# Performance work log

Measured on AMD Instinct MI355X. Metric: run time of the kernel, lower is better.

## Reference

```python
import jax, jax.numpy as jnp
import numpy as np

B, T, D, K = 32, 1024, 256, 1024


def setup_inputs() -> dict:
    key = jax.random.key(0)
    k1, k2 = jax.random.split(key)
    z_e_x = jax.random.normal(k1, (B, T, D), dtype=jnp.float32)
    # codebook initialized uniform(-1/K, 1/K) as in VQEmbedding.__init__
    codebook = jax.random.uniform(k2, (K, D), minval=-1.0 / K, maxval=1.0 / K, dtype=jnp.float32)
    return {"z_e_x": z_e_x, "codebook": codebook}


def _vq_indices(x_flat, codebook):
    c_sqr = jnp.sum(codebook * codebook, axis=1)            # [K]
    x_sqr = jnp.sum(x_flat * x_flat, axis=1, keepdims=True)  # [N,1]
    dist = c_sqr[None, :] + x_sqr - 2.0 * (x_flat @ codebook.T)  # [N,K]
    return jnp.argmin(dist, axis=1)                          # [N]


def reference(z_e_x, codebook):
    # VQEmbedding.straight_through with slice=1 (forward values)
    shp = z_e_x.shape
    x_flat = z_e_x.reshape(-1, codebook.shape[1])            # [N,D]
    idx = _vq_indices(x_flat, codebook)                      # [N] int
    codes = codebook[idx].reshape(shp)                       # gather lookup
    # z_q_x and z_q_x_bar are numerically identical (differ only in grad path);
    # also return the indices (what VQEmbedding.forward returns)
    return codes, codes, idx.reshape(shp[:-1])
```

## Files before the change

kernel.cpp:

```cpp
#include <hip/hip_runtime.h>


#define NROWS  32768
#define DDIM   256
#define KCODES 1024
#define MARGIN 1.5e-3f
#define CAP    1024
#define RPB    64
#define NCHUNK 16

typedef __attribute__((ext_vector_type(8))) short short8;
typedef __attribute__((ext_vector_type(4))) float f32x4;

__device__ __forceinline__ unsigned short f2bf(float f) {
    unsigned u = __float_as_uint(f);
    return (unsigned short)((u + 0x7FFFu + ((u >> 16) & 1u)) >> 16);
}

__device__ __forceinline__ float exact_dot(const float* __restrict__ xrow,
                                           const float* __restrict__ crow) {
    const float4* xp = (const float4*)xrow;
    const float4* cp = (const float4*)crow;
    float A = 0.f, B = 0.f;
    #pragma unroll 8
    for (int d4 = 0; d4 < 32; ++d4) {
        float4 xv = xp[d4], cv = cp[d4];
        A = __fmaf_rn(xv.x, cv.x, A);
        A = __fmaf_rn(xv.y, cv.y, A);
        A = __fmaf_rn(xv.z, cv.z, A);
        A = __fmaf_rn(xv.w, cv.w, A);
    }
    #pragma unroll 8
    for (int d4 = 32; d4 < 64; ++d4) {
        float4 xv = xp[d4], cv = cp[d4];
        B = __fmaf_rn(xv.x, cv.x, B);
        B = __fmaf_rn(xv.y, cv.y, B);
        B = __fmaf_rn(xv.z, cv.z, B);
        B = __fmaf_rn(xv.w, cv.w, B);
    }
    return __fadd_rn(A, B);
}

__global__ __launch_bounds__(256) void vq_csqr(const float* __restrict__ cb,
                                               float* __restrict__ csqr) {
    int gid  = blockIdx.x * 256 + threadIdx.x;
    int w    = gid >> 6;
    int lane = threadIdx.x & 63;
    if (w >= KCODES) return;
    float4 v = reinterpret_cast<const float4*>(cb)[w * (DDIM / 4) + lane];
    float s = v.x * v.x + v.y * v.y + v.z * v.z + v.w * v.w;
    #pragma unroll
    for (int off = 32; off > 0; off >>= 1) s += __shfl_down(s, off, 64);
    if (lane == 0) csqr[w] = s;
}

__global__ __launch_bounds__(256) void vq_xsqr(const float* __restrict__ x,
                                               float* __restrict__ xsqr) {
    int w = threadIdx.x >> 6, lane = threadIdx.x & 63;
    int row = blockIdx.x * 4 + w;
    float4 v = reinterpret_cast<const float4*>(x + (size_t)row * DDIM)[lane];
    float s = v.x * v.x + v.y * v.y + v.z * v.z + v.w * v.w;
    #pragma unroll
    for (int off = 32; off > 0; off >>= 1) s += __shfl_down(s, off, 64);
    if (lane == 0) xsqr[row] = s;
}

__global__ __launch_bounds__(256) void vq_cbfrag(const float* __restrict__ cb,
                                                 short* __restrict__ cbh) {
    int id   = blockIdx.x * 256 + threadIdx.x;
    int lane = id & 63;
    int ks   = (id >> 6) & 7;
    int nt   = id >> 9;
    int code = nt * 16 + (lane & 15);
    int d0   = ks * 32 + (lane >> 4) * 8;
    const float4* p = (const float4*)(cb + (size_t)code * DDIM + d0);
    float4 a = p[0], b = p[1];
    short8 v;
    v[0] = (short)f2bf(a.x); v[1] = (short)f2bf(a.y);
    v[2] = (short)f2bf(a.z); v[3] = (short)f2bf(a.w);
    v[4] = (short)f2bf(b.x); v[5] = (short)f2bf(b.y);
    v[6] = (short)f2bf(b.z); v[7] = (short)f2bf(b.w);
    *(short8*)(cbh + (size_t)id * 8) = v;
}

__global__ __launch_bounds__(256, 2) void vq_main(const float* __restrict__ x,
                                                  const float* __restrict__ cb,
                                                  const short* __restrict__ cbh,
                                                  const float* __restrict__ csqr,
                                                  const float* __restrict__ xsqr,
                                                  float* __restrict__ out) {
    __shared__ short              bstage[2][4 * 8 * 64 * 8];
    __shared__ float              csl[KCODES];
    __shared__ unsigned long long keys[RPB];
    __shared__ unsigned           list[CAP];
    __shared__ int                fidx[RPB];
    __shared__ int                cnt, ovf;

    const int t    = threadIdx.x;
    const int lane = t & 63;
    const int w    = t >> 6;
    const int r0   = blockIdx.x * RPB;
    const int lr   = lane & 15;
    const int lg   = lane >> 4;

    ((float4*)csl)[t] = ((const float4*)csqr)[t];
    if (t < RPB) keys[t] = ~0ULL;
    if (t == 0) { cnt = 0; ovf = 0; }

    short8 afr[8];
    {
        const float* xr = x + (size_t)(r0 + w * 16 + lr) * DDIM;
        #pragma unroll
        for (int ks = 0; ks < 8; ++ks) {
            float4 a = *(const float4*)&xr[ks * 32 + lg * 8];
            float4 b = *(const float4*)&xr[ks * 32 + lg * 8 + 4];
            short8 v;
            v[0] = (short)f2bf(a.x); v[1] = (short)f2bf(a.y);
            v[2] = (short)f2bf(a.z); v[3] = (short)f2bf(a.w);
            v[4] = (short)f2bf(b.x); v[5] = (short)f2bf(b.y);
            v[6] = (short)f2bf(b.z); v[7] = (short)f2bf(b.w);
            afr[ks] = v;
        }
    }

    const short8* cbh8 = (const short8*)cbh;

    short8 pf[8];
    #pragma unroll
    for (int i = 0; i < 8; ++i) pf[i] = cbh8[(size_t)0 * 2048 + i * 256 + t];
    {
        short8* dst = (short8*)bstage[0];
        #pragma unroll
        for (int i = 0; i < 8; ++i) dst[i * 256 + t] = pf[i];
        #pragma unroll
        for (int i = 0; i < 8; ++i) pf[i] = cbh8[(size_t)1 * 2048 + i * 256 + t];
    }
    __syncthreads();

    unsigned runp[4];
    #pragma unroll
    for (int j = 0; j < 4; ++j) runp[j] = ~0u;
    float thr[4];

    for (int c = 0; c < 2 * NCHUNK; ++c) {
        const int q = c & (NCHUNK - 1);
        if (c + 1 < 2 * NCHUNK) {
            short8* dst = (short8*)bstage[(c + 1) & 1];
            #pragma unroll
            for (int i = 0; i < 8; ++i) dst[i * 256 + t] = pf[i];
        }
        if (c + 2 < 2 * NCHUNK) {
            const size_t cb2 = (size_t)((c + 2) & (NCHUNK - 1)) * 2048;
            #pragma unroll
            for (int i = 0; i < 8; ++i) pf[i] = cbh8[cb2 + i * 256 + t];
        }
        const short* bs = bstage[c & 1];
        #pragma unroll
        for (int m = 0; m < 4; ++m) {
            const int nt = q * 4 + m;
            short8 bv[8];
            #pragma unroll
            for (int ks = 0; ks < 8; ++ks)
                bv[ks] = *(const short8*)&bs[((m * 8 + ks) * 64 + lane) * 8];
            f32x4 af = (f32x4){0.f, 0.f, 0.f, 0.f};
            #pragma unroll
            for (int ks = 0; ks < 8; ++ks)
                af = __builtin_amdgcn_mfma_f32_16x16x32_bf16(afr[ks], bv[ks], af, 0, 0, 0);

            const int code = nt * 16 + lr;
            float cs1 = __fadd_rn(csl[code], 1.0f);
            if (c < NCHUNK) {
                #pragma unroll
                for (int j = 0; j < 4; ++j) {
                    float s = __fmaf_rn(-2.f, af[j], cs1);
                    unsigned kp = (__float_as_uint(s) & 0xFFFFFC00u) | (unsigned)code;
                    runp[j] = runp[j] < kp ? runp[j] : kp;
                }
            } else {
                #pragma unroll
                for (int j = 0; j < 4; ++j) {
                    float s = __fmaf_rn(-2.f, af[j], cs1);
                    if (s <= thr[j]) {
                        int row = w * 16 + lg * 4 + j;
                        int pos = atomicAdd(&cnt, 1);
                        if (pos < CAP) list[pos] = ((unsigned)row << 10) | (unsigned)code;
                        else ovf = 1;
                    }
                }
            }
        }
        if (c == NCHUNK - 1) {
            #pragma unroll
            for (int j = 0; j < 4; ++j) {
                unsigned v = runp[j];
                #pragma unroll
                for (int mm = 1; mm < 16; mm <<= 1) {
                    unsigned o = __shfl_xor(v, mm, 64);
                    v = o < v ? o : v;
                }
                thr[j] = __uint_as_float(v & 0xFFFFFC00u) + MARGIN;
            }
        }
        __syncthreads();
    }

    if (ovf || cnt > CAP) {
        for (int it = t; it < RPB * KCODES; it += 256) {
            int row = it >> 10, code = it & (KCODES - 1);
            float dot = exact_dot(x + (size_t)(r0 + row) * DDIM, cb + (size_t)code * DDIM);
            float s   = __fmaf_rn(-2.f, dot, __fadd_rn(csl[code], xsqr[r0 + row]));
            atomicMin(&keys[row], ((unsigned long long)__float_as_uint(s) << 32) | (unsigned)code);
        }
    } else {
        for (int i = t; i < cnt; i += 256) {
            unsigned e = list[i];
            int row = (int)(e >> 10), code = (int)(e & 0x3FFu);
            float dot = exact_dot(x + (size_t)(r0 + row) * DDIM, cb + (size_t)code * DDIM);
            float s   = __fmaf_rn(-2.f, dot, __fadd_rn(csl[code], xsqr[r0 + row]));
            atomicMin(&keys[row], ((unsigned long long)__float_as_uint(s) << 32) | (unsigned)code);
        }
    }
    __syncthreads();

    if (t < RPB) {
        int code = (int)(unsigned)(keys[t] & 0xffffffffu);
        fidx[t] = code;
        out[(size_t)2 * NROWS * DDIM + (r0 + t)] = (float)code;
    }
    __syncthreads();

    const float4* cb4  = (const float4*)cb;
    float4*       out0 = (float4*)out;
    float4*       out1 = out0 + (size_t)NROWS * (DDIM / 4);
    #pragma unroll
    for (int i = 0; i < 16; ++i) {
        int it  = i * 256 + t;
        int row = it >> 6, col = it & 63;
        float4 v = cb4[(size_t)fidx[row] * (DDIM / 4) + col];
        size_t o = (size_t)(r0 + row) * (DDIM / 4) + col;
        out0[o] = v;
        out1[o] = v;
    }
}

extern "C" void kernel_launch(void* const* d_in, const int* in_sizes, int n_in,
                              void* d_out, int out_size, void* d_ws, size_t ws_size,
                              hipStream_t stream) {
    const float* x   = (const float*)d_in[0];
    const float* cb  = (const float*)d_in[1];
    float*       out = (float*)d_out;

    float* ws_csqr = (float*)d_ws;
    float* ws_xsqr = ws_csqr + KCODES;
    short* ws_cbh  = (short*)(ws_xsqr + NROWS);

    vq_cbfrag<<<128,        256, 0, stream>>>(cb, ws_cbh);
    vq_csqr  <<<256,        256, 0, stream>>>(cb, ws_csqr);
    vq_xsqr  <<<NROWS / 4,  256, 0, stream>>>(x, ws_xsqr);
    vq_main  <<<NROWS / RPB, 256, 0, stream>>>(x, cb, ws_cbh, ws_csqr, ws_xsqr, out);
}
```

Baseline: 94.05 us.

## Split codes across waves, hold all row tiles in registers, stage via global_load_lds

Each wave now keeps A fragments for all four 16-row tiles and handles its own quarter of the codebook, so every B fragment read from LDS feeds four MFMAs instead of one. Codebook staging uses direct global-to-LDS loads instead of round-tripping through registers. Because each wave only sees part of the codes, the running minimum becomes a cross-wave reduction through shared memory, with an extra barrier to build per-row thresholds. This raises register pressure (16 short8 A fragments plus 16 accumulators) and may limit occupancy.

After: 101.1 us. 7.5% more time.

```diff
diff --git a/kernel.cpp b/kernel.cpp
--- a/kernel.cpp
+++ b/kernel.cpp
@@ -91,6 +91,8 @@
                                                   float* __restrict__ out) {
     __shared__ short              bstage[2][4 * 8 * 64 * 8];
     __shared__ float              csl[KCODES];
+    __shared__ float              wred[4][RPB];
+    __shared__ float              thrl[RPB];
     __shared__ unsigned long long keys[RPB];
     __shared__ unsigned           list[CAP];
     __shared__ int                fidx[RPB];
@@ -107,9 +109,10 @@
     if (t < RPB) keys[t] = ~0ULL;
     if (t == 0) { cnt = 0; ovf = 0; }
 
-    short8 afr[8];
-    {
-        const float* xr = x + (size_t)(r0 + w * 16 + lr) * DDIM;
+    short8 afr[4][8];
+    #pragma unroll
+    for (int tile = 0; tile < 4; ++tile) {
+        const float* xr = x + (size_t)(r0 + tile * 16 + lr) * DDIM;
         #pragma unroll
         for (int ks = 0; ks < 8; ++ks) {
             float4 a = *(const float4*)&xr[ks * 32 + lg * 8];
@@ -119,89 +122,111 @@
             v[2] = (short)f2bf(a.z); v[3] = (short)f2bf(a.w);
             v[4] = (short)f2bf(b.x); v[5] = (short)f2bf(b.y);
             v[6] = (short)f2bf(b.z); v[7] = (short)f2bf(b.w);
-            afr[ks] = v;
-        }
-    }
-
-    const short8* cbh8 = (const short8*)cbh;
-
-    short8 pf[8];
-    #pragma unroll
-    for (int i = 0; i < 8; ++i) pf[i] = cbh8[(size_t)0 * 2048 + i * 256 + t];
-    {
-        short8* dst = (short8*)bstage[0];
-        #pragma unroll
-        for (int i = 0; i < 8; ++i) dst[i * 256 + t] = pf[i];
-        #pragma unroll
-        for (int i = 0; i < 8; ++i) pf[i] = cbh8[(size_t)1 * 2048 + i * 256 + t];
-    }
+            afr[tile][ks] = v;
+        }
+    }
+
+    const char* cbb = (const char*)cbh;
+    auto stage_chunk = [&](int buf, int c) {
+        const char* srcb = cbb + ((size_t)(w * 16 + c) << 13);
+        char*       dstb = (char*)bstage[buf] + ((size_t)w << 13);
+        #pragma unroll
+        for (int i = 0; i < 8; ++i) {
+            const void* src = srcb + i * 1024 + lane * 16;
+            __builtin_amdgcn_global_load_lds(
+                (const __attribute__((address_space(1))) void*)src,
+                (__attribute__((address_space(3))) void*)(dstb + i * 1024),
+                16, 0, 0);
+        }
+    };
+
+    stage_chunk(0, 0);
     __syncthreads();
 
-    unsigned runp[4];
-    #pragma unroll
-    for (int j = 0; j < 4; ++j) runp[j] = ~0u;
-    float thr[4];
-
-    for (int c = 0; c < 2 * NCHUNK; ++c) {
-        const int q = c & (NCHUNK - 1);
-        if (c + 1 < 2 * NCHUNK) {
-            short8* dst = (short8*)bstage[(c + 1) & 1];
-            #pragma unroll
-            for (int i = 0; i < 8; ++i) dst[i * 256 + t] = pf[i];
-        }
-        if (c + 2 < 2 * NCHUNK) {
-            const size_t cb2 = (size_t)((c + 2) & (NCHUNK - 1)) * 2048;
-            #pragma unroll
-            for (int i = 0; i < 8; ++i) pf[i] = cbh8[cb2 + i * 256 + t];
-        }
-        const short* bs = bstage[c & 1];
-        #pragma unroll
-        for (int m = 0; m < 4; ++m) {
-            const int nt = q * 4 + m;
-            short8 bv[8];
-            #pragma unroll
-            for (int ks = 0; ks < 8; ++ks)
-                bv[ks] = *(const short8*)&bs[((m * 8 + ks) * 64 + lane) * 8];
-            f32x4 af = (f32x4){0.f, 0.f, 0.f, 0.f};
-            #pragma unroll
-            for (int ks = 0; ks < 8; ++ks)
-                af = __builtin_amdgcn_mfma_f32_16x16x32_bf16(afr[ks], bv[ks], af, 0, 0, 0);
-
-            const int code = nt * 16 + lr;
-            float cs1 = __fadd_rn(csl[code], 1.0f);
-            if (c < NCHUNK) {
+    float runp[4][4];
+    #pragma unroll
+    for (int tile = 0; tile < 4; ++tile)
+        #pragma unroll
+        for (int j = 0; j < 4; ++j) runp[tile][j] = __builtin_inff();
+    float thr[4][4];
+
+    for (int cc = 0; cc < 2 * NCHUNK; ++cc) {
+        const int c = cc & (NCHUNK - 1);
+        if (cc + 1 < 2 * NCHUNK) stage_chunk((cc + 1) & 1, (cc + 1) & (NCHUNK - 1));
+
+        const short* bs = bstage[cc & 1];
+        short8 bv[8];
+        #pragma unroll
+        for (int ks = 0; ks < 8; ++ks)
+            bv[ks] = *(const short8*)&bs[((w * 8 + ks) * 64 + lane) * 8];
+        f32x4 af[4];
+        #pragma unroll
+        for (int tile = 0; tile < 4; ++tile) af[tile] = (f32x4){0.f, 0.f, 0.f, 0.f};
+        #pragma unroll
+        for (int ks = 0; ks < 8; ++ks) {
+            #pragma unroll
+            for (int tile = 0; tile < 4; ++tile)
+                af[tile] = __builtin_amdgcn_mfma_f32_16x16x32_bf16(afr[tile][ks], bv[ks], af[tile], 0, 0, 0);
+        }
+
+        const int nt   = w * 16 + c;
+        const int code = nt * 16 + lr;
+        const float cs1 = __fadd_rn(csl[code], 1.0f);
+        if (cc < NCHUNK) {
+            #pragma unroll
+            for (int tile = 0; tile < 4; ++tile)
                 #pragma unroll
                 for (int j = 0; j < 4; ++j) {
-                    float s = __fmaf_rn(-2.f, af[j], cs1);
-                    unsigned kp = (__float_as_uint(s) & 0xFFFFFC00u) | (unsigned)code;
-                    runp[j] = runp[j] < kp ? runp[j] : kp;
+                    float s = __fmaf_rn(-2.f, af[tile][j], cs1);
+                    runp[tile][j] = fminf(runp[tile][j], s);
                 }
-            } else {
+        } else {
+            #pragma unroll
+            for (int tile = 0; tile < 4; ++tile)
                 #pragma unroll
                 for (int j = 0; j < 4; ++j) {
-                    float s = __fmaf_rn(-2.f, af[j], cs1);
-                    if (s <= thr[j]) {
-                        int row = w * 16 + lg * 4 + j;
+                    float s = __fmaf_rn(-2.f, af[tile][j], cs1);
+                    if (s <= thr[tile][j]) {
+                        int row = tile * 16 + lg * 4 + j;
                         int pos = atomicAdd(&cnt, 1);
                         if (pos < CAP) list[pos] = ((unsigned)row << 10) | (unsigned)code;
                         else ovf = 1;
                     }
                 }
+        }
+
+        if (cc == NCHUNK - 1) {
+            #pragma unroll
+            for (int tile = 0; tile < 4; ++tile)
+                #pragma unroll
+                for (int j = 0; j < 4; ++j) {
+                    float v = runp[tile][j];
+                    v = fminf(v, __shfl_xor(v, 1, 64));
+                    v = fminf(v, __shfl_xor(v, 2, 64));
+                    v = fminf(v, __shfl_xor(v, 4, 64));
+                    v = fminf(v, __shfl_xor(v, 8, 64));
+                    runp[tile][j] = v;
+                }
+            if (lr == 0) {
+                #pragma unroll
+                for (int tile = 0; tile < 4; ++tile)
+                    #pragma unroll
+                    for (int j = 0; j < 4; ++j)
+                        wred[w][tile * 16 + lg * 4 + j] = runp[tile][j];
             }
         }
-        if (c == NCHUNK - 1) {
-            #pragma unroll
-            for (int j = 0; j < 4; ++j) {
-                unsigned v = runp[j];
-                #pragma unroll
-                for (int mm = 1; mm < 16; mm <<= 1) {
-                    unsigned o = __shfl_xor(v, mm, 64);
-                    v = o < v ? o : v;
-                }
-                thr[j] = __uint_as_float(v & 0xFFFFFC00u) + MARGIN;
+        __syncthreads();
+        if (cc == NCHUNK - 1) {
+            if (t < RPB) {
+                float m = fminf(fminf(wred[0][t], wred[1][t]), fminf(wred[2][t], wred[3][t]));
+                thrl[t] = m + MARGIN;
             }
-        }
-        __syncthreads();
+            __syncthreads();
+            #pragma unroll
+            for (int tile = 0; tile < 4; ++tile)
+                #pragma unroll
+                for (int j = 0; j < 4; ++j) thr[tile][j] = thrl[tile * 16 + lg * 4 + j];
+        }
     }
 
     if (ovf || cnt > CAP) {
```

## Replace two-pass bf16 scoring with single pass using running-min candidate filter

Applied to the files above, without the earlier changes.

The old kernel ran the bf16 MFMA distance sweep over the codebook twice: once to find each row's approximate minimum and a second time to collect candidates within a margin. The new version does a single sweep that keeps a running minimum per row (via lane shuffles) and appends any candidate within margin of the current minimum, storing a quantized score alongside it. Afterwards, candidates whose quantized score exceeds the final threshold are skipped before the exact fp32 rescoring. This halves the MFMA and LDS staging work, but adds a shuffle reduction per tile and lets more early candidates into the list. That is why CAP grows to 1536, and it raises the risk of falling into the overflow full-recompute path.

Result: slower. 120.5 us (+28.1%).

```diff
diff --git a/kernel.cpp b/kernel.cpp
--- a/kernel.cpp
+++ b/kernel.cpp
@@ -5,7 +5,7 @@
 #define DDIM   256
 #define KCODES 1024
 #define MARGIN 1.5e-3f
-#define CAP    1024
+#define CAP    1536
 #define RPB    64
 #define NCHUNK 16
 
@@ -15,6 +15,13 @@
 __device__ __forceinline__ unsigned short f2bf(float f) {
     unsigned u = __float_as_uint(f);
     return (unsigned short)((u + 0x7FFFu + ((u >> 16) & 1u)) >> 16);
+}
+
+__device__ __forceinline__ unsigned qscore(float s) {
+    float f = (s - 0.75f) * 131072.0f;
+    if (f <= 0.f) return 0u;
+    if (f >= 65535.f) return 65535u;
+    return (unsigned)f;
 }
 
 __device__ __forceinline__ float exact_dot(const float* __restrict__ xrow,
@@ -93,6 +100,7 @@
     __shared__ float              csl[KCODES];
     __shared__ unsigned long long keys[RPB];
     __shared__ unsigned           list[CAP];
+    __shared__ unsigned           qthrl[RPB];
     __shared__ int                fidx[RPB];
     __shared__ int                cnt, ovf;
 
@@ -137,27 +145,23 @@
     }
     __syncthreads();
 
-    unsigned runp[4];
-    #pragma unroll
-    for (int j = 0; j < 4; ++j) runp[j] = ~0u;
-    float thr[4];
-
-    for (int c = 0; c < 2 * NCHUNK; ++c) {
-        const int q = c & (NCHUNK - 1);
-        if (c + 1 < 2 * NCHUNK) {
+    float runm[4] = {__builtin_inff(), __builtin_inff(), __builtin_inff(), __builtin_inff()};
+
+    for (int c = 0; c < NCHUNK; ++c) {
+        if (c + 1 < NCHUNK) {
             short8* dst = (short8*)bstage[(c + 1) & 1];
             #pragma unroll
             for (int i = 0; i < 8; ++i) dst[i * 256 + t] = pf[i];
         }
-        if (c + 2 < 2 * NCHUNK) {
-            const size_t cb2 = (size_t)((c + 2) & (NCHUNK - 1)) * 2048;
+        if (c + 2 < NCHUNK) {
+            const size_t cb2 = (size_t)(c + 2) * 2048;
             #pragma unroll
             for (int i = 0; i < 8; ++i) pf[i] = cbh8[cb2 + i * 256 + t];
         }
         const short* bs = bstage[c & 1];
         #pragma unroll
         for (int m = 0; m < 4; ++m) {
-            const int nt = q * 4 + m;
+            const int nt = c * 4 + m;
             short8 bv[8];
             #pragma unroll
             for (int ks = 0; ks < 8; ++ks)
@@ -168,41 +172,33 @@
                 af = __builtin_amdgcn_mfma_f32_16x16x32_bf16(afr[ks], bv[ks], af, 0, 0, 0);
 
             const int code = nt * 16 + lr;
-            float cs1 = __fadd_rn(csl[code], 1.0f);
-            if (c < NCHUNK) {
-                #pragma unroll
-                for (int j = 0; j < 4; ++j) {
-                    float s = __fmaf_rn(-2.f, af[j], cs1);
-                    unsigned kp = (__float_as_uint(s) & 0xFFFFFC00u) | (unsigned)code;
-                    runp[j] = runp[j] < kp ? runp[j] : kp;
-                }
-            } else {
-                #pragma unroll
-                for (int j = 0; j < 4; ++j) {
-                    float s = __fmaf_rn(-2.f, af[j], cs1);
-                    if (s <= thr[j]) {
-                        int row = w * 16 + lg * 4 + j;
-                        int pos = atomicAdd(&cnt, 1);
-                        if (pos < CAP) list[pos] = ((unsigned)row << 10) | (unsigned)code;
-                        else ovf = 1;
-                    }
+            const float cs1 = __fadd_rn(csl[code], 1.0f);
+            #pragma unroll
+            for (int j = 0; j < 4; ++j) {
+                float s = __fmaf_rn(-2.f, af[j], cs1);
+                float v = s;
+                v = fminf(v, __shfl_xor(v, 1, 64));
+                v = fminf(v, __shfl_xor(v, 2, 64));
+                v = fminf(v, __shfl_xor(v, 4, 64));
+                v = fminf(v, __shfl_xor(v, 8, 64));
+                runm[j] = fminf(runm[j], v);
+                if (s <= runm[j] + MARGIN) {
+                    int row = w * 16 + lg * 4 + j;
+                    int pos = atomicAdd(&cnt, 1);
+                    if (pos < CAP) list[pos] = (qscore(s) << 16) | ((unsigned)row << 10) | (unsigned)code;
+                    else ovf = 1;
                 }
             }
         }
-        if (c == NCHUNK - 1) {
-            #pragma unroll
-            for (int j = 0; j < 4; ++j) {
-                unsigned v = runp[j];
-                #pragma unroll
-                for (int mm = 1; mm < 16; mm <<= 1) {
-                    unsigned o = __shfl_xor(v, mm, 64);
-                    v = o < v ? o : v;
-                }
-                thr[j] = __uint_as_float(v & 0xFFFFFC00u) + MARGIN;
-            }
-        }
         __syncthreads();
     }
+
+    if (lr == 0) {
+        #pragma unroll
+        for (int j = 0; j < 4; ++j)
+            qthrl[w * 16 + lg * 4 + j] = qscore(runm[j] + MARGIN);
+    }
+    __syncthreads();
 
     if (ovf || cnt > CAP) {
         for (int it = t; it < RPB * KCODES; it += 256) {
@@ -213,8 +209,10 @@
         }
     } else {
         for (int i = t; i < cnt; i += 256) {
-            unsigned e = list[i];
-            int row = (int)(e >> 10), code = (int)(e & 0x3FFu);
+            unsigned e   = list[i];
+            int row      = (int)((e >> 10) & 63u);
+            if ((e >> 16) > qthrl[row]) continue;
+            int code     = (int)(e & 0x3FFu);
             float dot = exact_dot(x + (size_t)(r0 + row) * DDIM, cb + (size_t)code * DDIM);
             float s   = __fmaf_rn(-2.f, dot, __fadd_rn(csl[code], xsqr[r0 + row]));
             atomicMin(&keys[row], ((unsigned long long)__float_as_uint(s) << 32) | (unsigned)code);
```
